# Performance work log

Hardware: AMD Instinct MI355X
Metric: run time of the kernel (lower is better)

## Reference

```python
import jax, jax.numpy as jnp
import numpy as np
import math

D_MODEL = 256
N_HEADS = 4
D_HEAD = D_MODEL // N_HEADS  # 64
TT_RANK = 4
BATCH = 4
SEQ = 2048


def _xavier(key, shape):
    fan_in, fan_out = shape[0], shape[-1]
    if len(shape) == 4:  # (H, d, d, r) treated roughly like dense xavier
        fan_in, fan_out = shape[1], shape[2] * shape[3]
    lim = math.sqrt(6.0 / (fan_in + fan_out))
    return jax.random.uniform(key, shape, jnp.float32, -lim, lim)


def setup_inputs() -> dict:
    key = jax.random.key(0)
    ks = jax.random.split(key, 12)
    inp = {
        "query": jax.random.normal(ks[0], (BATCH, SEQ, D_MODEL), jnp.float32),
        "key": jax.random.normal(ks[1], (BATCH, SEQ, D_MODEL), jnp.float32),
        "value": jax.random.normal(ks[2], (BATCH, SEQ, D_MODEL), jnp.float32),
        "Wq": _xavier(ks[3], (D_MODEL, D_MODEL)),
        "bq": jnp.zeros((D_MODEL,), jnp.float32),
        "Wk": _xavier(ks[4], (D_MODEL, D_MODEL)),
        "bk": jnp.zeros((D_MODEL,), jnp.float32),
        "Wv": _xavier(ks[5], (D_MODEL, D_MODEL)),
        "bv": jnp.zeros((D_MODEL,), jnp.float32),
        "W2": _xavier(ks[6], (N_HEADS, D_HEAD, D_HEAD, TT_RANK)),
        "alpha": jnp.float32(0.5),  # nonzero so interaction path is exercised
        "Wo": _xavier(ks[7], (D_MODEL, D_MODEL)),
        "bo": jnp.zeros((D_MODEL,), jnp.float32),
    }
    return inp


def reference(query, key, value, Wq, bq, Wk, bk, Wv, bv, W2, alpha, Wo, bo):
    B, Sq, _ = query.shape
    Sk = key.shape[1]
    H, Dh = N_HEADS, D_HEAD

    # projections -> (B, H, S, Dh)
    Q = (query @ Wq + bq).reshape(B, Sq, H, Dh).transpose(0, 2, 1, 3)
    K = (key @ Wk + bk).reshape(B, Sk, H, Dh).transpose(0, 2, 1, 3)
    V = (value @ Wv + bv).reshape(B, Sk, H, Dh).transpose(0, 2, 1, 3)

    scale = math.sqrt(Dh)
    scores = jnp.einsum('bhqd,bhkd->bhqk', Q, K) / scale  # (B,H,Sq,Sk)

    # rank-2 tensor interaction: Qp[b,h,q,a,r] = sum_d Q[b,h,q,d] W2[h,d,a,r]
    #                            Kp[b,h,k,a,r] = sum_e K[b,h,k,e] W2[h,a,e,r]
    Qp = jnp.einsum('bhqd,hdar->bhqar', Q, W2)
    Kp = jnp.einsum('bhke,haer->bhkar', K, W2)
    interaction = jnp.einsum('bhqar,bhkar->bhqk', Qp, Kp) / (Dh * scale)

    total_scores = scores + alpha * interaction
    attn = jax.nn.softmax(total_scores, axis=-1)

    out = jnp.einsum('bhqk,bhkd->bhqd', attn, V)
    out = out.transpose(0, 2, 1, 3).reshape(B, Sq, H * Dh)
    return out @ Wo + bo
```

## Files before the change

### kernel.cpp

```cpp
#include <hip/hip_runtime.h>
#include <hip/hip_bf16.h>

#define BB   4
#define SS   2048
#define DM   256
#define HH   4
#define DHH  64
#define KSPL 4
#define KLEN (SS / KSPL)

typedef unsigned short ushort_t;
typedef unsigned int   uint_t;
using short8   = __attribute__((ext_vector_type(8))) short;
using ushort8  = __attribute__((ext_vector_type(8))) unsigned short;
using ushort4v = __attribute__((ext_vector_type(4))) unsigned short;
using float4v  = __attribute__((ext_vector_type(4))) float;

__device__ __forceinline__ ushort_t f2bf(float f) {
  uint_t u = __float_as_uint(f);
  uint_t r = (u + 0x7FFFu + ((u >> 16) & 1u)) >> 16;
  return (ushort_t)r;
}

__global__ __launch_bounds__(256) void k_pre(
    const float* __restrict__ Wk, const float* __restrict__ Wv,
    const float* __restrict__ Wo, const float* __restrict__ Wq,
    const float* __restrict__ bq, const float* __restrict__ W2,
    const float* __restrict__ alpha_p,
    ushort_t* __restrict__ WkT, ushort_t* __restrict__ WvT,
    ushort_t* __restrict__ WoT, ushort_t* __restrict__ WcT,
    float* __restrict__ bc) {
  __shared__ float sT[64 * 65];
  __shared__ __align__(16) float sM[64];
  const int t = threadIdx.x;
  const int bi = blockIdx.x;
  if (bi < 48) {
    int m = bi >> 4, tile = bi & 15;
    int ot = tile >> 2, ct = tile & 3;
    const float* src = (m == 0) ? Wk : (m == 1) ? Wv : Wo;
    ushort_t* dst = (m == 0) ? WkT : (m == 1) ? WvT : WoT;
#pragma unroll
    for (int it = 0; it < 16; ++it) {
      int i = it * 4 + (t >> 6), j = t & 63;
      sT[i * 65 + j] = src[(ct * 64 + i) * 256 + ot * 64 + j];
    }
    __syncthreads();
#pragma unroll
    for (int it = 0; it < 16; ++it) {
      int jj = it * 4 + (t >> 6), ii = t & 63;
      dst[(ot * 64 + jj) * 256 + ct * 64 + ii] = f2bf(sT[ii * 65 + jj]);
    }
  } else {
    int o = bi - 48;
    int h = o >> 6, e = o & 63;
    if (t < 64) {
      const float* Wd = W2 + h * 16384 + t * 256;
      const float* We = W2 + h * 16384 + e * 4;
      float s = 0.f;
#pragma unroll 8
      for (int a = 0; a < 64; ++a) {
        float4 x = *(const float4*)(Wd + a * 4);
        float4 y = *(const float4*)(We + a * 256);
        s += x.x * y.x + x.y * y.y + x.z * y.z + x.w * y.w;
      }
      sM[t] = (t == e ? 0.125f : 0.f) + alpha_p[0] * (1.f / 512.f) * s;
    }
    __syncthreads();
    const float* Wrow = Wq + t * 256 + h * 64;
    float s = 0.f;
#pragma unroll
    for (int d4 = 0; d4 < 16; ++d4) {
      float4 x = *(const float4*)(Wrow + d4 * 4);
      float4 mm = *(const float4*)(sM + d4 * 4);
      s += x.x * mm.x + x.y * mm.y + x.z * mm.z + x.w * mm.w;
    }
    WcT[o * 256 + t] = f2bf(s);
    if (t == 0) {
      float sb = 0.f;
      for (int d = 0; d < 64; ++d) sb += bq[h * 64 + d] * sM[d];
      bc[o] = sb;
    }
  }
}

template <int MODE>
__device__ __forceinline__ void pgemm(
    const ushort_t* __restrict__ sX, const ushort_t* __restrict__ WT,
    const float* __restrict__ bias, int w, int g, int l16,
    int b, int s0, ushort_t* __restrict__ dst) {
  float4v acc[2];
  acc[0] = (float4v){0.f, 0.f, 0.f, 0.f};
  acc[1] = (float4v){0.f, 0.f, 0.f, 0.f};
#pragma unroll
  for (int kc = 0; kc < 8; ++kc) {
    short8 af = *(const short8*)&sX[l16 * 256 + (((kc * 4 + g) ^ (l16 & 7)) << 3)];
#pragma unroll
    for (int ct = 0; ct < 2; ++ct) {
      int col = w * 32 + ct * 16 + l16;
      short8 bf = *(const short8*)&WT[col * 256 + kc * 32 + g * 8];
      acc[ct] = __builtin_amdgcn_mfma_f32_16x16x32_bf16(af, bf, acc[ct], 0, 0, 0);
    }
  }
#pragma unroll
  for (int ct = 0; ct < 2; ++ct) {
    int col = w * 32 + ct * 16 + l16;
    float bv = bias[col];
    int h = col >> 6, d = col & 63;
    if (MODE == 1) {
      ushort4v pk;
#pragma unroll
      for (int r = 0; r < 4; ++r) pk[r] = f2bf(acc[ct][r] + bv);
      *(ushort4v*)&dst[((size_t)(b * HH + h) * DHH + d) * SS + s0 + g * 4] = pk;
    } else {
#pragma unroll
      for (int r = 0; r < 4; ++r)
        dst[((size_t)(b * HH + h) * SS + s0 + g * 4 + r) * DHH + d] =
            f2bf(acc[ct][r] + bv);
    }
  }
}

__global__ __launch_bounds__(512) void k_proj(
    const float* __restrict__ q_in, const float* __restrict__ k_in,
    const float* __restrict__ v_in,
    const float* __restrict__ bk, const float* __restrict__ bv,
    const ushort_t* __restrict__ WcT, const ushort_t* __restrict__ WkT,
    const ushort_t* __restrict__ WvT, const float* __restrict__ bc,
    ushort_t* __restrict__ Qa, ushort_t* __restrict__ Ka,
    ushort_t* __restrict__ VTg) {
  __shared__ ushort_t sXq[16 * 256];
  __shared__ ushort_t sXk[16 * 256];
  __shared__ ushort_t sXv[16 * 256];

  const int t = threadIdx.x;
  const int w = t >> 6, lane = t & 63, g = lane >> 4, l16 = lane & 15;
  const int row0 = blockIdx.x * 16;
  const int b = row0 >> 11, s0 = row0 & (SS - 1);

  {
    int r = t >> 5, cf = (t & 31) * 8;
    int sw = r * 256 + (((cf >> 3) ^ (r & 7)) << 3);
    const float* qp = q_in + (size_t)(row0 + r) * DM + cf;
    const float* kp = k_in + (size_t)(row0 + r) * DM + cf;
    const float* vp = v_in + (size_t)(row0 + r) * DM + cf;
    float4 a0 = *(const float4*)qp, a1 = *(const float4*)(qp + 4);
    float4 b0 = *(const float4*)kp, b1 = *(const float4*)(kp + 4);
    float4 c0 = *(const float4*)vp, c1 = *(const float4*)(vp + 4);
    ushort8 uq, uk, uv;
    uq[0] = f2bf(a0.x); uq[1] = f2bf(a0.y); uq[2] = f2bf(a0.z); uq[3] = f2bf(a0.w);
    uq[4] = f2bf(a1.x); uq[5] = f2bf(a1.y); uq[6] = f2bf(a1.z); uq[7] = f2bf(a1.w);
    uk[0] = f2bf(b0.x); uk[1] = f2bf(b0.y); uk[2] = f2bf(b0.z); uk[3] = f2bf(b0.w);
    uk[4] = f2bf(b1.x); uk[5] = f2bf(b1.y); uk[6] = f2bf(b1.z); uk[7] = f2bf(b1.w);
    uv[0] = f2bf(c0.x); uv[1] = f2bf(c0.y); uv[2] = f2bf(c0.z); uv[3] = f2bf(c0.w);
    uv[4] = f2bf(c1.x); uv[5] = f2bf(c1.y); uv[6] = f2bf(c1.z); uv[7] = f2bf(c1.w);
    *(ushort8*)&sXq[sw] = uq;
    *(ushort8*)&sXk[sw] = uk;
    *(ushort8*)&sXv[sw] = uv;
  }
  __syncthreads();

  pgemm<0>(sXq, WcT, bc, w, g, l16, b, s0, Qa);
  pgemm<0>(sXk, WkT, bk, w, g, l16, b, s0, Ka);
  pgemm<1>(sXv, WvT, bv, w, g, l16, b, s0, VTg);
}

__global__ __launch_bounds__(256, 4) void k_attn(
    const ushort_t* __restrict__ Qa, const ushort_t* __restrict__ Ka,
    const ushort_t* __restrict__ VTg,
    float* __restrict__ Opart, float* __restrict__ lpart) {
  __shared__ ushort_t sKa[64 * 64];
  __shared__ ushort_t sVT[64 * 64];
  __shared__ ushort_t sPT[128 * 64];

  const int t = threadIdx.x;
  const int w = t >> 6, lane = t & 63, g = lane >> 4, l16 = lane & 15;
  const int bh = blockIdx.y;
  const int q0 = blockIdx.x * 128;
  const int ks = blockIdx.z;

  short8 qfrag[2][2];
#pragma unroll
  for (int s = 0; s < 2; ++s) {
    const ushort_t* qp =
        Qa + ((size_t)bh * SS + q0 + s * 64 + w * 16 + l16) * DHH + g * 8;
    qfrag[s][0] = *(const short8*)(qp);
    qfrag[s][1] = *(const short8*)(qp + 32);
  }

  const ushort_t* KaB = Ka + (size_t)bh * SS * DHH + (size_t)ks * KLEN * DHH;
  const ushort_t* VTB = VTg + (size_t)bh * DHH * SS + ks * KLEN;

  const int r0 = t >> 3, c0 = t & 7, r1 = r0 + 32;
  const int sw0 = r0 * 64 + ((c0 ^ (r0 & 7)) << 3);
  const int sw1 = r1 * 64 + ((c0 ^ (r1 & 7)) << 3);

  float l_run[2] = {0.f, 0.f};
  float4v oacc[2][4];
#pragma unroll
  for (int s = 0; s < 2; ++s)
#pragma unroll
    for (int dj = 0; dj < 4; ++dj) oacc[s][dj] = (float4v){0.f, 0.f, 0.f, 0.f};

  for (int kch = 0; kch < KLEN / 64; ++kch) {
    __syncthreads();
    {
      short8 k0 = *(const short8*)(KaB + (size_t)(kch * 64 + r0) * DHH + c0 * 8);
      short8 k1 = *(const short8*)(KaB + (size_t)(kch * 64 + r1) * DHH + c0 * 8);
      short8 v0 = *(const short8*)(VTB + (size_t)r0 * SS + kch * 64 + c0 * 8);
      short8 v1 = *(const short8*)(VTB + (size_t)r1 * SS + kch * 64 + c0 * 8);
      *(short8*)(sKa + sw0) = k0;
      *(short8*)(sKa + sw1) = k1;
      *(short8*)(sVT + sw0) = v0;
      *(short8*)(sVT + sw1) = v1;
    }
    __syncthreads();

    float4v sacc[2][4];
#pragma unroll
    for (int s = 0; s < 2; ++s)
#pragma unroll
      for (int kj = 0; kj < 4; ++kj)
        sacc[s][kj] = (float4v){-20.f, -20.f, -20.f, -20.f};
#pragma unroll
    for (int kc = 0; kc < 2; ++kc) {
#pragma unroll
      for (int kj = 0; kj < 4; ++kj) {
        int krow = kj * 16 + l16;
        short8 kf = *(const short8*)(sKa + krow * 64 +
                                     (((kc * 4 + g) ^ (krow & 7)) << 3));
        sacc[0][kj] = __builtin_amdgcn_mfma_f32_16x16x32_bf16(
            kf, qfrag[0][kc], sacc[0][kj], 0, 0, 0);
        sacc[1][kj] = __builtin_amdgcn_mfma_f32_16x16x32_bf16(
            kf, qfrag[1][kc], sacc[1][kj], 0, 0, 0);
      }
    }

#pragma unroll
    for (int s = 0; s < 2; ++s) {
      int qrow = s * 64 + w * 16 + l16;
      float lp = 0.f;
#pragma unroll
      for (int kj = 0; kj < 4; ++kj) {
        float p0 = __expf(sacc[s][kj][0]);
        float p1 = __expf(sacc[s][kj][1]);
        float p2 = __expf(sacc[s][kj][2]);
        float p3 = __expf(sacc[s][kj][3]);
        uint_t u01 = __builtin_amdgcn_perm(__float_as_uint(p1),
                                           __float_as_uint(p0), 0x07060302u);
        uint_t u23 = __builtin_amdgcn_perm(__float_as_uint(p3),
                                           __float_as_uint(p2), 0x07060302u);
        lp += __uint_as_float(__float_as_uint(p0) & 0xFFFF0000u);
        lp += __uint_as_float(__float_as_uint(p1) & 0xFFFF0000u);
        lp += __uint_as_float(__float_as_uint(p2) & 0xFFFF0000u);
        lp += __uint_as_float(__float_as_uint(p3) & 0xFFFF0000u);
        int kbase = kj * 16 + g * 4;
        uint2 pack; pack.x = u01; pack.y = u23;
        *(uint2*)(sPT + qrow * 64 + (((kbase >> 3) ^ (qrow & 7)) << 3) +
                  (kbase & 7)) = pack;
      }
      l_run[s] += lp;
    }

#pragma unroll
    for (int ck = 0; ck < 2; ++ck) {
      short8 vb[4];
#pragma unroll
      for (int dj = 0; dj < 4; ++dj) {
        int vrow = dj * 16 + l16;
        vb[dj] = *(const short8*)(sVT + vrow * 64 +
                                  (((ck * 4 + g) ^ (vrow & 7)) << 3));
      }
#pragma unroll
      for (int s = 0; s < 2; ++s) {
        int qrow = s * 64 + w * 16 + l16;
        short8 pa = *(const short8*)(sPT + qrow * 64 +
                                     (((ck * 4 + g) ^ (qrow & 7)) << 3));
#pragma unroll
        for (int dj = 0; dj < 4; ++dj)
          oacc[s][dj] = __builtin_amdgcn_mfma_f32_16x16x32_bf16(
              pa, vb[dj], oacc[s][dj], 0, 0, 0);
      }
    }
  }

  const int b = bh >> 2, h = bh & 3;
  float* Ob = Opart + (size_t)ks * (8192 * 256);
#pragma unroll
  for (int s = 0; s < 2; ++s) {
    l_run[s] += __shfl_xor(l_run[s], 16, 64);
    l_run[s] += __shfl_xor(l_run[s], 32, 64);
    if (g == 0)
      lpart[(size_t)ks * (8192 * 4) +
            ((size_t)b * SS + q0 + s * 64 + w * 16 + l16) * 4 + h] = l_run[s];
#pragma unroll
    for (int r = 0; r < 4; ++r) {
      size_t row = (size_t)b * SS + q0 + s * 64 + w * 16 + g * 4 + r;
#pragma unroll
      for (int dj = 0; dj < 4; ++dj)
        Ob[row * DM + h * DHH + dj * 16 + l16] = oacc[s][dj][r];
    }
  }
}

__global__ __launch_bounds__(512) void k_out(
    const float* __restrict__ Opart, const float* __restrict__ lpart,
    const ushort_t* __restrict__ WoT, const float* __restrict__ bo,
    float* __restrict__ Out) {
  __shared__ ushort_t sA[16 * 256];
  const int t = threadIdx.x;
  const int w = t >> 6, lane = t & 63, g = lane >> 4, l16 = lane & 15;
  const int row0 = blockIdx.x * 16;
  {
    int r = t >> 5, cf = (t & 31) * 8;
    size_t row = row0 + r;
    int h = cf >> 6;
    float l = 0.f;
    float s0 = 0.f, s1 = 0.f, s2 = 0.f, s3 = 0.f,
          s4 = 0.f, s5 = 0.f, s6 = 0.f, s7 = 0.f;
#pragma unroll
    for (int ks = 0; ks < KSPL; ++ks) {
      l += lpart[(size_t)ks * (8192 * 4) + row * 4 + h];
      const float* o = Opart + (size_t)ks * (8192 * 256) + row * DM + cf;
      float4 a0 = *(const float4*)o, a1 = *(const float4*)(o + 4);
      s0 += a0.x; s1 += a0.y; s2 += a0.z; s3 += a0.w;
      s4 += a1.x; s5 += a1.y; s6 += a1.z; s7 += a1.w;
    }
    float linv = 1.0f / l;
    ushort8 u;
    u[0] = f2bf(s0 * linv); u[1] = f2bf(s1 * linv);
    u[2] = f2bf(s2 * linv); u[3] = f2bf(s3 * linv);
    u[4] = f2bf(s4 * linv); u[5] = f2bf(s5 * linv);
    u[6] = f2bf(s6 * linv); u[7] = f2bf(s7 * linv);
    *(ushort8*)&sA[r * 256 + (((cf >> 3) ^ (r & 7)) << 3)] = u;
  }
  __syncthreads();

  float4v acc[2];
  acc[0] = (float4v){0.f, 0.f, 0.f, 0.f};
  acc[1] = (float4v){0.f, 0.f, 0.f, 0.f};
#pragma unroll
  for (int kc = 0; kc < 8; ++kc) {
    short8 af = *(const short8*)&sA[l16 * 256 + (((kc * 4 + g) ^ (l16 & 7)) << 3)];
#pragma unroll
    for (int ct = 0; ct < 2; ++ct) {
      int col = w * 32 + ct * 16 + l16;
      short8 bf = *(const short8*)&WoT[col * 256 + kc * 32 + g * 8];
      acc[ct] = __builtin_amdgcn_mfma_f32_16x16x32_bf16(af, bf, acc[ct], 0, 0, 0);
    }
  }
#pragma unroll
  for (int ct = 0; ct < 2; ++ct) {
    int col = w * 32 + ct * 16 + l16;
    float bv = bo[col];
#pragma unroll
    for (int r = 0; r < 4; ++r)
      Out[(size_t)(row0 + g * 4 + r) * DM + col] = acc[ct][r] + bv;
  }
}

extern "C" void kernel_launch(void* const* d_in, const int* in_sizes, int n_in,
                              void* d_out, int out_size, void* d_ws, size_t ws_size,
                              hipStream_t stream) {
  (void)in_sizes; (void)n_in; (void)out_size; (void)ws_size;
  const float* q_in  = (const float*)d_in[0];
  const float* k_in  = (const float*)d_in[1];
  const float* v_in  = (const float*)d_in[2];
  const float* Wq    = (const float*)d_in[3];
  const float* bq    = (const float*)d_in[4];
  const float* Wk    = (const float*)d_in[5];
  const float* bk    = (const float*)d_in[6];
  const float* Wv    = (const float*)d_in[7];
  const float* bv    = (const float*)d_in[8];
  const float* W2    = (const float*)d_in[9];
  const float* alpha = (const float*)d_in[10];
  const float* Wo    = (const float*)d_in[11];
  const float* bo    = (const float*)d_in[12];
  float* out = (float*)d_out;

  char* ws = (char*)d_ws;
  ushort_t* Qa    = (ushort_t*)ws;
  ushort_t* Ka    = (ushort_t*)(ws + 4194304);
  ushort_t* VTg   = (ushort_t*)(ws + 8388608);
  float*    Opart = (float*)(ws + 12582912);
  float*    lpart = (float*)(ws + 46137344);
  ushort_t* WkT   = (ushort_t*)(ws + 48234496);
  ushort_t* WvT   = (ushort_t*)(ws + 48365568);
  ushort_t* WoT   = (ushort_t*)(ws + 48496640);
  ushort_t* WcT   = (ushort_t*)(ws + 48627712);
  float*    bc    = (float*)(ws + 48758784);

  hipLaunchKernelGGL(k_pre, dim3(304), dim3(256), 0, stream,
                     Wk, Wv, Wo, Wq, bq, W2, alpha, WkT, WvT, WoT, WcT, bc);
  hipLaunchKernelGGL(k_proj, dim3(512), dim3(512), 0, stream,
                     q_in, k_in, v_in, bk, bv, WcT, WkT, WvT, bc, Qa, Ka, VTg);
  hipLaunchKernelGGL(k_attn, dim3(SS / 128, BB * HH, KSPL), dim3(256), 0,
                     stream, Qa, Ka, VTg, Opart, lpart);
  hipLaunchKernelGGL(k_out, dim3(512), dim3(512), 0, stream,
                     Opart, lpart, WoT, bo, out);
}
```

Measured before the change: 162.8 us.

## Drop key-split in attention, double-buffer K/V tiles, normalize and emit bf16 directly

Removes the 4-way split over the key dimension, so each 512-thread block (8 waves, 16 query rows each) walks all 2048 keys for a 128-row query tile. K/V tiles are register-prefetched two chunks ahead into double-buffered shared memory, which leaves one barrier per chunk. The attention kernel now divides by the row sum and writes a bf16 attention output, so the fp32 partial buffers and the reduction in the output-projection kernel go away. The trade-off is a grid of only 256 blocks with longer serial key loops, and a block-index swizzle that changes how (b,h) pairs are mapped.

```diff
diff --git a/kernel.cpp b/kernel.cpp
--- a/kernel.cpp
+++ b/kernel.cpp
@@ -6,8 +6,7 @@
 #define DM   256
 #define HH   4
 #define DHH  64
-#define KSPL 4
-#define KLEN (SS / KSPL)
+#define NCH  (SS / 64)
 
 typedef unsigned short ushort_t;
 typedef unsigned int   uint_t;
@@ -164,87 +163,79 @@
   pgemm<1>(sXv, WvT, bv, w, g, l16, b, s0, VTg);
 }
 
-__global__ __launch_bounds__(256, 4) void k_attn(
+__global__ __launch_bounds__(512) void k_attn(
     const ushort_t* __restrict__ Qa, const ushort_t* __restrict__ Ka,
-    const ushort_t* __restrict__ VTg,
-    float* __restrict__ Opart, float* __restrict__ lpart) {
-  __shared__ ushort_t sKa[64 * 64];
-  __shared__ ushort_t sVT[64 * 64];
+    const ushort_t* __restrict__ VTg, ushort_t* __restrict__ Abuf) {
+  __shared__ ushort_t sK[2][64 * 64];
+  __shared__ ushort_t sV[2][64 * 64];
   __shared__ ushort_t sPT[128 * 64];
 
   const int t = threadIdx.x;
   const int w = t >> 6, lane = t & 63, g = lane >> 4, l16 = lane & 15;
-  const int bh = blockIdx.y;
-  const int q0 = blockIdx.x * 128;
-  const int ks = blockIdx.z;
-
-  short8 qfrag[2][2];
-#pragma unroll
-  for (int s = 0; s < 2; ++s) {
+
+  const int id = blockIdx.x;
+  const int qt = (id >> 3) & 15;
+  const int bh = ((id & 7) << 1) | (id >> 7);
+  const int q0 = qt * 128;
+
+  short8 qfrag[2];
+  {
     const ushort_t* qp =
-        Qa + ((size_t)bh * SS + q0 + s * 64 + w * 16 + l16) * DHH + g * 8;
-    qfrag[s][0] = *(const short8*)(qp);
-    qfrag[s][1] = *(const short8*)(qp + 32);
-  }
-
-  const ushort_t* KaB = Ka + (size_t)bh * SS * DHH + (size_t)ks * KLEN * DHH;
-  const ushort_t* VTB = VTg + (size_t)bh * DHH * SS + ks * KLEN;
-
-  const int r0 = t >> 3, c0 = t & 7, r1 = r0 + 32;
-  const int sw0 = r0 * 64 + ((c0 ^ (r0 & 7)) << 3);
-  const int sw1 = r1 * 64 + ((c0 ^ (r1 & 7)) << 3);
-
-  float l_run[2] = {0.f, 0.f};
-  float4v oacc[2][4];
-#pragma unroll
-  for (int s = 0; s < 2; ++s)
-#pragma unroll
-    for (int dj = 0; dj < 4; ++dj) oacc[s][dj] = (float4v){0.f, 0.f, 0.f, 0.f};
-
-  for (int kch = 0; kch < KLEN / 64; ++kch) {
-    __syncthreads();
-    {
-      short8 k0 = *(const short8*)(KaB + (size_t)(kch * 64 + r0) * DHH + c0 * 8);
-      short8 k1 = *(const short8*)(KaB + (size_t)(kch * 64 + r1) * DHH + c0 * 8);
-      short8 v0 = *(const short8*)(VTB + (size_t)r0 * SS + kch * 64 + c0 * 8);
-      short8 v1 = *(const short8*)(VTB + (size_t)r1 * SS + kch * 64 + c0 * 8);
-      *(short8*)(sKa + sw0) = k0;
-      *(short8*)(sKa + sw1) = k1;
-      *(short8*)(sVT + sw0) = v0;
-      *(short8*)(sVT + sw1) = v1;
-    }
-    __syncthreads();
-
-    float4v sacc[2][4];
-#pragma unroll
-    for (int s = 0; s < 2; ++s)
-#pragma unroll
-      for (int kj = 0; kj < 4; ++kj)
-        sacc[s][kj] = (float4v){-20.f, -20.f, -20.f, -20.f};
+        Qa + ((size_t)bh * SS + q0 + w * 16 + l16) * DHH + g * 8;
+    qfrag[0] = *(const short8*)(qp);
+    qfrag[1] = *(const short8*)(qp + 32);
+  }
+
+  const ushort_t* KaB = Ka + (size_t)bh * SS * DHH;
+  const ushort_t* VTB = VTg + (size_t)bh * DHH * SS;
+
+  const int r0 = t >> 3, c0 = t & 7;
+  const int sw = r0 * 64 + ((c0 ^ (r0 & 7)) << 3);
+
+  short8 kreg = *(const short8*)(KaB + (size_t)r0 * DHH + c0 * 8);
+  short8 vreg = *(const short8*)(VTB + (size_t)r0 * SS + c0 * 8);
+  *(short8*)(sK[0] + sw) = kreg;
+  *(short8*)(sV[0] + sw) = vreg;
+  kreg = *(const short8*)(KaB + (size_t)(64 + r0) * DHH + c0 * 8);
+  vreg = *(const short8*)(VTB + (size_t)r0 * SS + 64 + c0 * 8);
+
+  float l_run = 0.f;
+  float4v oacc[4];
+#pragma unroll
+  for (int dj = 0; dj < 4; ++dj) oacc[dj] = (float4v){0.f, 0.f, 0.f, 0.f};
+  const int qrow = w * 16 + l16;
+
+  __syncthreads();
+
+  for (int kch = 0; kch < NCH; ++kch) {
+    const int cur = kch & 1;
+    const ushort_t* sKc = sK[cur];
+    const ushort_t* sVc = sV[cur];
+
+    float4v sacc[4];
+#pragma unroll
+    for (int kj = 0; kj < 4; ++kj)
+      sacc[kj] = (float4v){-20.f, -20.f, -20.f, -20.f};
 #pragma unroll
     for (int kc = 0; kc < 2; ++kc) {
 #pragma unroll
       for (int kj = 0; kj < 4; ++kj) {
         int krow = kj * 16 + l16;
-        short8 kf = *(const short8*)(sKa + krow * 64 +
+        short8 kf = *(const short8*)(sKc + krow * 64 +
                                      (((kc * 4 + g) ^ (krow & 7)) << 3));
-        sacc[0][kj] = __builtin_amdgcn_mfma_f32_16x16x32_bf16(
-            kf, qfrag[0][kc], sacc[0][kj], 0, 0, 0);
-        sacc[1][kj] = __builtin_amdgcn_mfma_f32_16x16x32_bf16(
-            kf, qfrag[1][kc], sacc[1][kj], 0, 0, 0);
-      }
-    }
-
-#pragma unroll
-    for (int s = 0; s < 2; ++s) {
-      int qrow = s * 64 + w * 16 + l16;
+        sacc[kj] = __builtin_amdgcn_mfma_f32_16x16x32_bf16(
+            kf, qfrag[kc], sacc[kj], 0, 0, 0);
+      }
+    }
+
+    {
       float lp = 0.f;
 #pragma unroll
       for (int kj = 0; kj < 4; ++kj) {
-        float p0 = __expf(sacc[s][kj][0]);
-        float p1 = __expf(sacc[s][kj][1]);
-        float p2 = __expf(sacc[s][kj][2]);
-        float p3 = __expf(sacc[s][kj][3]);
+        float p0 = __expf(sacc[kj][0]);
+        float p1 = __expf(sacc[kj][1]);
+        float p2 = __expf(sacc[kj][2]);
+        float p3 = __expf(sacc[kj][3]);
         uint_t u01 = __builtin_amdgcn_perm(__float_as_uint(p1),
                                            __float_as_uint(p0), 0x07060302u);
         uint_t u23 = __builtin_amdgcn_perm(__float_as_uint(p3),
@@ -258,7 +249,7 @@
         *(uint2*)(sPT + qrow * 64 + (((kbase >> 3) ^ (qrow & 7)) << 3) +
                   (kbase & 7)) = pack;
       }
-      l_run[s] += lp;
+      l_run += lp;
     }
 
 #pragma unroll
@@ -267,70 +258,57 @@
 #pragma unroll
       for (int dj = 0; dj < 4; ++dj) {
         int vrow = dj * 16 + l16;
-        vb[dj] = *(const short8*)(sVT + vrow * 64 +
+        vb[dj] = *(const short8*)(sVc + vrow * 64 +
                                   (((ck * 4 + g) ^ (vrow & 7)) << 3));
       }
-#pragma unroll
-      for (int s = 0; s < 2; ++s) {
-        int qrow = s * 64 + w * 16 + l16;
-        short8 pa = *(const short8*)(sPT + qrow * 64 +
-                                     (((ck * 4 + g) ^ (qrow & 7)) << 3));
-#pragma unroll
-        for (int dj = 0; dj < 4; ++dj)
-          oacc[s][dj] = __builtin_amdgcn_mfma_f32_16x16x32_bf16(
-              pa, vb[dj], oacc[s][dj], 0, 0, 0);
-      }
-    }
-  }
+      short8 pa = *(const short8*)(sPT + qrow * 64 +
+                                   (((ck * 4 + g) ^ (qrow & 7)) << 3));
+#pragma unroll
+      for (int dj = 0; dj < 4; ++dj)
+        oacc[dj] = __builtin_amdgcn_mfma_f32_16x16x32_bf16(
+            pa, vb[dj], oacc[dj], 0, 0, 0);
+    }
+
+    if (kch < NCH - 1) {
+      *(short8*)(sK[cur ^ 1] + sw) = kreg;
+      *(short8*)(sV[cur ^ 1] + sw) = vreg;
+      if (kch < NCH - 2) {
+        kreg = *(const short8*)(KaB + (size_t)((kch + 2) * 64 + r0) * DHH +
+                                c0 * 8);
+        vreg = *(const short8*)(VTB + (size_t)r0 * SS + (kch + 2) * 64 +
+                                c0 * 8);
+      }
+    }
+    __syncthreads();
+  }
+
+  l_run += __shfl_xor(l_run, 16, 64);
+  l_run += __shfl_xor(l_run, 32, 64);
+  float lrow[4];
+#pragma unroll
+  for (int r = 0; r < 4; ++r) lrow[r] = __shfl(l_run, g * 4 + r, 64);
 
   const int b = bh >> 2, h = bh & 3;
-  float* Ob = Opart + (size_t)ks * (8192 * 256);
-#pragma unroll
-  for (int s = 0; s < 2; ++s) {
-    l_run[s] += __shfl_xor(l_run[s], 16, 64);
-    l_run[s] += __shfl_xor(l_run[s], 32, 64);
-    if (g == 0)
-      lpart[(size_t)ks * (8192 * 4) +
-            ((size_t)b * SS + q0 + s * 64 + w * 16 + l16) * 4 + h] = l_run[s];
-#pragma unroll
-    for (int r = 0; r < 4; ++r) {
-      size_t row = (size_t)b * SS + q0 + s * 64 + w * 16 + g * 4 + r;
-#pragma unroll
-      for (int dj = 0; dj < 4; ++dj)
-        Ob[row * DM + h * DHH + dj * 16 + l16] = oacc[s][dj][r];
-    }
+#pragma unroll
+  for (int r = 0; r < 4; ++r) {
+    float linv = 1.0f / lrow[r];
+    size_t row = (size_t)b * SS + q0 + w * 16 + g * 4 + r;
+#pragma unroll
+    for (int dj = 0; dj < 4; ++dj)
+      Abuf[row * DM + h * DHH + dj * 16 + l16] = f2bf(oacc[dj][r] * linv);
   }
 }
 
 __global__ __launch_bounds__(512) void k_out(
-    const float* __restrict__ Opart, const float* __restrict__ lpart,
-    const ushort_t* __restrict__ WoT, const float* __restrict__ bo,
-    float* __restrict__ Out) {
+    const ushort_t* __restrict__ Abuf, const ushort_t* __restrict__ WoT,
+    const float* __restrict__ bo, float* __restrict__ Out) {
   __shared__ ushort_t sA[16 * 256];
   const int t = threadIdx.x;
   const int w = t >> 6, lane = t & 63, g = lane >> 4, l16 = lane & 15;
   const int row0 = blockIdx.x * 16;
   {
     int r = t >> 5, cf = (t & 31) * 8;
-    size_t row = row0 + r;
-    int h = cf >> 6;
-    float l = 0.f;
-    float s0 = 0.f, s1 = 0.f, s2 = 0.f, s3 = 0.f,
-          s4 = 0.f, s5 = 0.f, s6 = 0.f, s7 = 0.f;
-#pragma unroll
-    for (int ks = 0; ks < KSPL; ++ks) {
-      l += lpart[(size_t)ks * (8192 * 4) + row * 4 + h];
-      const float* o = Opart + (size_t)ks * (8192 * 256) + row * DM + cf;
-      float4 a0 = *(const float4*)o, a1 = *(const float4*)(o + 4);
-      s0 += a0.x; s1 += a0.y; s2 += a0.z; s3 += a0.w;
-      s4 += a1.x; s5 += a1.y; s6 += a1.z; s7 += a1.w;
-    }
-    float linv = 1.0f / l;
-    ushort8 u;
-    u[0] = f2bf(s0 * linv); u[1] = f2bf(s1 * linv);
-    u[2] = f2bf(s2 * linv); u[3] = f2bf(s3 * linv);
-    u[4] = f2bf(s4 * linv); u[5] = f2bf(s5 * linv);
-    u[6] = f2bf(s6 * linv); u[7] = f2bf(s7 * linv);
+    ushort8 u = *(const ushort8*)(Abuf + (size_t)(row0 + r) * DM + cf);
     *(ushort8*)&sA[r * 256 + (((cf >> 3) ^ (r & 7)) << 3)] = u;
   }
   __syncthreads();
@@ -378,23 +356,22 @@
   float* out = (float*)d_out;
 
   char* ws = (char*)d_ws;
-  ushort_t* Qa    = (ushort_t*)ws;
-  ushort_t* Ka    = (ushort_t*)(ws + 4194304);
-  ushort_t* VTg   = (ushort_t*)(ws + 8388608);
-  float*    Opart = (float*)(ws + 12582912);
-  float*    lpart = (float*)(ws + 46137344);
-  ushort_t* WkT   = (ushort_t*)(ws + 48234496);
-  ushort_t* WvT   = (ushort_t*)(ws + 48365568);
-  ushort_t* WoT   = (ushort_t*)(ws + 48496640);
-  ushort_t* WcT   = (ushort_t*)(ws + 48627712);
-  float*    bc    = (float*)(ws + 48758784);
+  ushort_t* Qa   = (ushort_t*)ws;
+  ushort_t* Ka   = (ushort_t*)(ws + 4194304);
+  ushort_t* VTg  = (ushort_t*)(ws + 8388608);
+  ushort_t* Abuf = (ushort_t*)(ws + 12582912);
+  ushort_t* WkT  = (ushort_t*)(ws + 16777216);
+  ushort_t* WvT  = (ushort_t*)(ws + 16908288);
+  ushort_t* WoT  = (ushort_t*)(ws + 17039360);
+  ushort_t* WcT  = (ushort_t*)(ws + 17170432);
+  float*    bc   = (float*)(ws + 17301504);
 
   hipLaunchKernelGGL(k_pre, dim3(304), dim3(256), 0, stream,
                      Wk, Wv, Wo, Wq, bq, W2, alpha, WkT, WvT, WoT, WcT, bc);
   hipLaunchKernelGGL(k_proj, dim3(512), dim3(512), 0, stream,
                      q_in, k_in, v_in, bk, bv, WcT, WkT, WvT, bc, Qa, Ka, VTg);
-  hipLaunchKernelGGL(k_attn, dim3(SS / 128, BB * HH, KSPL), dim3(256), 0,
-                     stream, Qa, Ka, VTg, Opart, lpart);
+  hipLaunchKernelGGL(k_attn, dim3(256), dim3(512), 0, stream,
+                     Qa, Ka, VTg, Abuf);
   hipLaunchKernelGGL(k_out, dim3(512), dim3(512), 0, stream,
-                     Opart, lpart, WoT, bo, out);
-}
+                     Abuf, WoT, bo, out);
+}
```

Measured after the change: 159.9 us. No clear change (-1.8%).
